# Kernel optimization log

Hardware: AMD Instinct MI355X
Metric: run time of the kernel (lower is better)

Reference implementation:

```python
import jax, jax.numpy as jnp
import numpy as np
import math

B, D, NH, HD, FF, P, IMG = 4, 768, 12, 64, 3072, 16, 256
L = (IMG // P) ** 2      # 256 tokens
PD = P * P * 3           # 768 patch dim
GRID = IMG // P          # 16


def setup_inputs() -> dict:
    key = jax.random.key(0)
    ks = iter(jax.random.split(key, 80))
    def nrm(shape, s=0.02):
        return jax.random.normal(next(ks), shape, jnp.float32) * s
    return {
        "x": jax.random.normal(next(ks), (B, 3, IMG, IMG), jnp.float32),
        "pe_norm_w": jnp.ones((PD,), jnp.float32),
        "pe_proj_w": nrm((PD, D)),
        "pe_proj_b": jnp.zeros((D,), jnp.float32),
        "pe_norm_out_w": jnp.ones((D,), jnp.float32),
        "pos_embed": nrm((1, L, D)),
        "in_attn_norm_w": jnp.ones((6, D), jnp.float32),
        "in_qkv_w": nrm((6, D, 3 * D)),
        "in_out_w": nrm((6, D, D)),
        "in_ff_norm_w": jnp.ones((6, D), jnp.float32),
        "in_w1": nrm((6, D, 2 * FF)),
        "in_w2": nrm((6, FF, D)),
        "mid_attn_norm_w": jnp.ones((3, D), jnp.float32),
        "mid_qkv_w": nrm((3, D, 3 * D)),
        "mid_out_w": nrm((3, D, D)),
        "mid_ff_norm_w": jnp.ones((3, D), jnp.float32),
        "mid_w1": nrm((3, D, 2 * FF)),
        "mid_w2": nrm((3, FF, D)),
        "out_skip_w": nrm((2 * D, D)),
        "out_skip_b": jnp.zeros((D,), jnp.float32),
        "out_attn_norm_w": jnp.ones((D,), jnp.float32),
        "out_qkv_w": nrm((D, 3 * D)),
        "out_out_w": nrm((D, D)),
        "out_ff_norm_w": jnp.ones((D,), jnp.float32),
        "out_w1": nrm((D, 2 * FF)),
        "out_w2": nrm((FF, D)),
        "final_norm_w": jnp.ones((D,), jnp.float32),
        "ol_proj_w": nrm((D, PD)),
        "ol_proj_b": jnp.zeros((PD,), jnp.float32),
        "rb_conv_in_w": nrm((128, 3, 3, 3), 0.1),
        "rb_gn_w": jnp.ones((5, 128), jnp.float32),
        "rb_gn_b": jnp.zeros((5, 128), jnp.float32),
        "rb_conv1_w": nrm((128, 1, 5, 5), 0.1),
        "rb_conv2_w": nrm((128, 1, 5, 5), 0.1),
        "head_conv_w": nrm((1, 128, 3, 3), 0.1),
    }


def _mish(x):
    return x * jnp.tanh(jax.nn.softplus(x))


def _rms(x, w, eps=1e-5):
    return x * jax.lax.rsqrt(jnp.mean(x * x, axis=-1, keepdims=True) + eps) * w


def _attn(x, qkv_w, out_w):
    b, l, _ = x.shape
    q, k, v = jnp.split(x @ qkv_w, 3, axis=-1)
    s = 1.0 / math.sqrt(HD)  # applied to BOTH q and k, as in source
    q = (q * s).reshape(b, l, NH, HD)
    k = (k * s).reshape(b, l, NH, HD)
    v = v.reshape(b, l, NH, HD)
    logits = jnp.einsum('bqhd,bkhd->bhqk', q, k).astype(jnp.float32)
    w = jax.nn.softmax(logits, axis=-1).astype(x.dtype)
    o = jnp.einsum('bhqk,bkhd->bqhd', w, v).reshape(b, l, NH * HD)
    return o @ out_w


def _ff(x, w1, w2):
    a, g = jnp.split(x @ w1, 2, axis=-1)
    return (_mish(a) * g) @ w2


def _block(x, an, qkv, ow, fn, w1, w2):
    x = x + _attn(_rms(x, an), qkv, ow)
    x = x + _ff(_rms(x, fn), w1, w2)
    return x


def _gn(x, w, b, groups=8, eps=1e-5):
    bb, c, h, ww = x.shape
    xg = x.reshape(bb, groups, c // groups, h, ww)
    m = jnp.mean(xg, axis=(2, 3, 4), keepdims=True)
    v = jnp.var(xg, axis=(2, 3, 4), keepdims=True)
    xn = ((xg - m) * jax.lax.rsqrt(v + eps)).reshape(bb, c, h, ww)
    return xn * w[:, None, None] + b[:, None, None]


def _conv(x, w, pad, dil=1, groups=1):
    xp = jnp.pad(x, ((0, 0), (0, 0), (pad, pad), (pad, pad)), mode='reflect')
    return jax.lax.conv_general_dilated(
        xp, w, window_strides=(1, 1), padding='VALID', rhs_dilation=(dil, dil),
        feature_group_count=groups, dimension_numbers=('NCHW', 'OIHW', 'NCHW'))


def _forward(x, pe_norm_w, pe_proj_w, pe_proj_b, pe_norm_out_w, pos_embed,
             in_attn_norm_w, in_qkv_w, in_out_w, in_ff_norm_w, in_w1, in_w2,
             mid_attn_norm_w, mid_qkv_w, mid_out_w, mid_ff_norm_w, mid_w1, mid_w2,
             out_skip_w, out_skip_b, out_attn_norm_w, out_qkv_w, out_out_w,
             out_ff_norm_w, out_w1, out_w2, final_norm_w, ol_proj_w, ol_proj_b,
             rb_conv_in_w, rb_gn_w, rb_gn_b, rb_conv1_w, rb_conv2_w, head_conv_w):
    b = x.shape[0]
    # PatchEmbed: b c (h p1) (w p2) -> b (h w) (p1 p2 c)
    t = x.reshape(b, 3, GRID, P, GRID, P).transpose(0, 2, 4, 3, 5, 1).reshape(b, L, PD)
    t = _rms(t, pe_norm_w)
    t = t @ pe_proj_w + pe_proj_b
    t = _rms(t, pe_norm_out_w)
    t = t + pos_embed
    # U-ViT trunk: 6 in blocks (skips saved), 3 middle, 1 out block (source typo -> single out block)
    skips = []
    for i in range(6):
        t = _block(t, in_attn_norm_w[i], in_qkv_w[i], in_out_w[i],
                   in_ff_norm_w[i], in_w1[i], in_w2[i])
        skips.append(t)
    for i in range(3):
        t = _block(t, mid_attn_norm_w[i], mid_qkv_w[i], mid_out_w[i],
                   mid_ff_norm_w[i], mid_w1[i], mid_w2[i])
    t = jnp.concatenate([t, skips[-1]], axis=-1) @ out_skip_w + out_skip_b
    t = _block(t, out_attn_norm_w, out_qkv_w, out_out_w, out_ff_norm_w, out_w1, out_w2)
    t = _rms(t, final_norm_w)
    # OutBlock: proj, dropout(eval=identity), unpatchify to b 3 256 256
    t = t @ ol_proj_w + ol_proj_b
    img = t.reshape(b, GRID, GRID, P, P, 3).transpose(0, 5, 1, 3, 2, 4).reshape(b, 3, IMG, IMG)
    # ResNetBlock(128)
    h = _conv(img, rb_conv_in_w, 1)
    h = _mish(_gn(h, rb_gn_w[0], rb_gn_b[0]))
    res = h
    h = _mish(_gn(_conv(h, rb_conv1_w, 2, 1, 128), rb_gn_w[1], rb_gn_b[1]))
    h = res + h
    h = _mish(_gn(h, rb_gn_w[2], rb_gn_b[2]))
    res = h
    h = _mish(_gn(_conv(h, rb_conv2_w, 6, 3, 128), rb_gn_w[3], rb_gn_b[3]))
    h = res + h
    h = _mish(_gn(h, rb_gn_w[4], rb_gn_b[4]))
    return _conv(h, head_conv_w, 1)  # [B, 1, 256, 256]


def reference(x, pe_norm_w, pe_proj_w, pe_proj_b, pe_norm_out_w, pos_embed,
              in_attn_norm_w, in_qkv_w, in_out_w, in_ff_norm_w, in_w1, in_w2,
              mid_attn_norm_w, mid_qkv_w, mid_out_w, mid_ff_norm_w, mid_w1, mid_w2,
              out_skip_w, out_skip_b, out_attn_norm_w, out_qkv_w, out_out_w,
              out_ff_norm_w, out_w1, out_w2, final_norm_w, ol_proj_w, ol_proj_b,
              rb_conv_in_w, rb_gn_w, rb_gn_b, rb_conv1_w, rb_conv2_w, head_conv_w):
    return _forward(x, pe_norm_w, pe_proj_w, pe_proj_b, pe_norm_out_w, pos_embed,
                    in_attn_norm_w, in_qkv_w, in_out_w, in_ff_norm_w, in_w1, in_w2,
                    mid_attn_norm_w, mid_qkv_w, mid_out_w, mid_ff_norm_w, mid_w1, mid_w2,
                    out_skip_w, out_skip_b, out_attn_norm_w, out_qkv_w, out_out_w,
                    out_ff_norm_w, out_w1, out_w2, final_norm_w, ol_proj_w, ol_proj_b,
                    rb_conv_in_w, rb_gn_w, rb_gn_b, rb_conv1_w, rb_conv2_w, head_conv_w)
```

## Files before the change

kernel.cpp:

```cpp
#include <hip/hip_runtime.h>
#include <math.h>

#define B_ 4
#define D_ 768
#define NH_ 12
#define HD_ 64
#define FF_ 3072
#define L_ 256
#define PD_ 768
#define GRID_ 16
#define P_ 16
#define IMG_ 256
#define M_ (B_*L_)
#define NCONV_ (B_*128*IMG_*IMG_)

typedef __attribute__((ext_vector_type(8))) short short8;
typedef __attribute__((ext_vector_type(4))) float f32x4;
typedef __attribute__((ext_vector_type(4))) unsigned short us4;
typedef __attribute__((ext_vector_type(8))) unsigned short us8;
typedef unsigned short ushort_t;

__device__ __forceinline__ float mishf(float x){
    float e = __expf(x);
    float u = (1.f + e) * (1.f + e);
    return x * (1.f - 2.f / (u + 1.f));
}

__device__ __forceinline__ int refl(int i, int n){
    if (i < 0) i = -i;
    if (i >= n) i = 2*n - 2 - i;
    return i;
}

__device__ __forceinline__ ushort_t f2bf(float f){
    unsigned int u = __float_as_uint(f);
    unsigned int r = (u + 0x7FFFu + ((u >> 16) & 1u)) >> 16;
    return (ushort_t)r;
}
__device__ __forceinline__ float bf2f(ushort_t u){
    return __uint_as_float(((unsigned int)u) << 16);
}

__device__ __forceinline__ void block_red2(float& s, float& q){
    #pragma unroll
    for (int o = 32; o > 0; o >>= 1){ s += __shfl_down(s, o); q += __shfl_down(q, o); }
    __shared__ float r1[4], r2[4];
    int tid = threadIdx.x;
    if ((tid & 63) == 0){ r1[tid>>6] = s; r2[tid>>6] = q; }
    __syncthreads();
    if (tid == 0){ s = r1[0]+r1[1]+r1[2]+r1[3]; q = r2[0]+r2[1]+r2[2]+r2[3]; }
    __syncthreads();
}

__global__ __launch_bounds__(256) void k_patchify(const float* __restrict__ x, float* __restrict__ t){
    int idx = blockIdx.x*256 + threadIdx.x;
    int d = idx % PD_; int l = (idx/PD_) % L_; int b = idx/(PD_*L_);
    int c = d % 3; int p = d / 3; int p1 = p / P_; int p2 = p % P_;
    int gh = l / GRID_; int gw = l % GRID_;
    int sy = gh*P_ + p1, sx = gw*P_ + p2;
    t[idx] = x[(((size_t)b*3 + c)*IMG_ + sy)*IMG_ + sx];
}

__global__ __launch_bounds__(256) void k_wt(const float* __restrict__ b0, const float* __restrict__ b1,
                                            const float* __restrict__ b2, int n0, int n1,
                                            ushort_t* __restrict__ dst, int K, int N){
    int z = blockIdx.z;
    size_t sz = (size_t)K * N;
    const float* src = (z < n0) ? b0 + (size_t)z*sz
                     : (z < n0+n1) ? b1 + (size_t)(z-n0)*sz
                     : b2 + (size_t)(z-n0-n1)*sz;
    ushort_t* out = dst + (size_t)z*sz;
    __shared__ float ld[32][33];
    int k0 = blockIdx.y*32, nc0 = blockIdx.x*32;
    int tid = threadIdx.x;
    int c = tid & 31, r8 = tid >> 5;
    #pragma unroll
    for (int i = 0; i < 4; ++i){
        int k = r8 + i*8;
        ld[k][c] = src[(size_t)(k0+k)*N + nc0 + c];
    }
    __syncthreads();
    #pragma unroll
    for (int i = 0; i < 4; ++i){
        int n = r8 + i*8;
        out[(size_t)(nc0+n)*K + k0 + c] = f2bf(ld[c][n]);
    }
}

template<bool OUT_BF>
__global__ __launch_bounds__(256) void k_rms(const float* __restrict__ x, const float* __restrict__ w,
                                             const float* __restrict__ addv, void* __restrict__ yv){
    int row = blockIdx.x;
    const float* xr = x + (size_t)row * D_;
    float s = 0.f;
    for (int i = threadIdx.x; i < D_; i += 256){ float v = xr[i]; s += v*v; }
    __shared__ float red[256];
    red[threadIdx.x] = s; __syncthreads();
    for (int o = 128; o > 0; o >>= 1){
        if (threadIdx.x < o) red[threadIdx.x] += red[threadIdx.x+o];
        __syncthreads();
    }
    float rstd = rsqrtf(red[0]/(float)D_ + 1e-5f);
    int l = row % L_;
    for (int i = threadIdx.x; i < D_; i += 256){
        float v = xr[i]*rstd*w[i];
        if (addv) v += addv[(size_t)l*D_ + i];
        if (OUT_BF) ((ushort_t*)yv)[(size_t)row*D_ + i] = f2bf(v);
        else        ((float*)yv)[(size_t)row*D_ + i] = v;
    }
}

__global__ __launch_bounds__(256) void k_skred_rms(const float* __restrict__ Pp, float* __restrict__ t,
                                                   const float* __restrict__ w, ushort_t* __restrict__ nb){
    int row = blockIdx.x;
    int tid = threadIdx.x;
    float v[3];
    float s = 0.f;
    #pragma unroll
    for (int i = 0; i < 3; ++i){
        int c = tid + i*256;
        size_t o = (size_t)row*D_ + c;
        float x = t[o] + Pp[o] + Pp[(size_t)M_*D_ + o];
        v[i] = x; s += x*x;
        t[o] = x;
    }
    #pragma unroll
    for (int o = 32; o > 0; o >>= 1) s += __shfl_down(s, o);
    __shared__ float r1[4];
    if ((tid & 63) == 0) r1[tid>>6] = s;
    __syncthreads();
    float tot = r1[0]+r1[1]+r1[2]+r1[3];
    float rstd = rsqrtf(tot*(1.f/768.f) + 1e-5f);
    if (w){
        #pragma unroll
        for (int i = 0; i < 3; ++i){
            int c = tid + i*256;
            nb[(size_t)row*D_ + c] = f2bf(v[i]*rstd*w[c]);
        }
    }
}

template<bool OBF, int SPLITK>
__global__ __launch_bounds__(256) void k_gemm(const ushort_t* __restrict__ A, const ushort_t* __restrict__ Wt,
                                              void* __restrict__ Cv, const float* __restrict__ bias,
                                              const float* __restrict__ res, int N, int K){
    __shared__ ushort_t As[2][64][40];
    __shared__ ushort_t Ws[2][64][40];
    int tid = threadIdx.x;
    int lane = tid & 63, wid = tid >> 6;
    int wr = wid >> 1, wc = wid & 1;
    int row0 = blockIdx.y * 64, col0 = blockIdx.x * 64;
    f32x4 acc[2][2];
    #pragma unroll
    for (int i = 0; i < 2; ++i)
        #pragma unroll
        for (int j = 0; j < 2; ++j) acc[i][j] = (f32x4){0.f,0.f,0.f,0.f};

    int lg = lane >> 4, lr = lane & 15;
    int sr = tid >> 2, sk = (tid & 3) * 8;
    int kc = K / SPLITK;
    int k0 = (SPLITK > 1) ? blockIdx.z * kc : 0;
    const ushort_t* arow = A  + (size_t)(row0 + sr)*K + k0 + sk;
    const ushort_t* wrow = Wt + (size_t)(col0 + sr)*K + k0 + sk;

    for (int kt = 0; kt < kc; kt += 64){
        __syncthreads();
        *(short8*)&As[0][sr][sk] = *(const short8*)(arow + kt);
        *(short8*)&As[1][sr][sk] = *(const short8*)(arow + kt + 32);
        *(short8*)&Ws[0][sr][sk] = *(const short8*)(wrow + kt);
        *(short8*)&Ws[1][sr][sk] = *(const short8*)(wrow + kt + 32);
        __syncthreads();
        short8 a0[2], a1[2], b0[2], b1[2];
        #pragma unroll
        for (int i = 0; i < 2; ++i){
            a0[i] = *(const short8*)(&As[0][wr*32 + i*16 + lr][lg*8]);
            a1[i] = *(const short8*)(&As[1][wr*32 + i*16 + lr][lg*8]);
        }
        #pragma unroll
        for (int j = 0; j < 2; ++j){
            b0[j] = *(const short8*)(&Ws[0][wc*32 + j*16 + lr][lg*8]);
            b1[j] = *(const short8*)(&Ws[1][wc*32 + j*16 + lr][lg*8]);
        }
        #pragma unroll
        for (int i = 0; i < 2; ++i)
            #pragma unroll
            for (int j = 0; j < 2; ++j){
                acc[i][j] = __builtin_amdgcn_mfma_f32_16x16x32_bf16(a0[i], b0[j], acc[i][j], 0, 0, 0);
                acc[i][j] = __builtin_amdgcn_mfma_f32_16x16x32_bf16(a1[i], b1[j], acc[i][j], 0, 0, 0);
            }
    }
    if (SPLITK > 1){
        float* Pp = (float*)Cv + (size_t)blockIdx.z * M_ * N;
        #pragma unroll
        for (int i = 0; i < 2; ++i)
            #pragma unroll
            for (int j = 0; j < 2; ++j)
                #pragma unroll
                for (int q = 0; q < 4; ++q){
                    int m = row0 + wr*32 + i*16 + lg*4 + q;
                    int n = col0 + wc*32 + j*16 + lr;
                    Pp[(size_t)m*N + n] = acc[i][j][q];
                }
    } else {
        #pragma unroll
        for (int i = 0; i < 2; ++i)
            #pragma unroll
            for (int j = 0; j < 2; ++j)
                #pragma unroll
                for (int q = 0; q < 4; ++q){
                    int m = row0 + wr*32 + i*16 + lg*4 + q;
                    int n = col0 + wc*32 + j*16 + lr;
                    float v = acc[i][j][q];
                    if (bias) v += bias[n];
                    size_t o = (size_t)m*N + n;
                    if (OBF){
                        ((ushort_t*)Cv)[o] = f2bf(v);
                    } else {
                        if (res) v += res[o];
                        ((float*)Cv)[o] = v;
                    }
                }
    }
}

__global__ __launch_bounds__(256) void k_gemm_glu(const ushort_t* __restrict__ A, const ushort_t* __restrict__ Wt,
                                                  ushort_t* __restrict__ Cb, int K){
    __shared__ ushort_t As[2][64][40];
    __shared__ ushort_t Wa[2][64][40];
    __shared__ ushort_t Wg[2][64][40];
    int tid = threadIdx.x;
    int lane = tid & 63, wid = tid >> 6;
    int wr = wid >> 1, wc = wid & 1;
    int row0 = blockIdx.y * 64, col0 = blockIdx.x * 64;
    f32x4 aa[2][2], ag[2][2];
    #pragma unroll
    for (int i = 0; i < 2; ++i)
        #pragma unroll
        for (int j = 0; j < 2; ++j){ aa[i][j] = (f32x4){0.f,0.f,0.f,0.f}; ag[i][j] = (f32x4){0.f,0.f,0.f,0.f}; }

    int lg = lane >> 4, lr = lane & 15;
    int sr = tid >> 2, sk = (tid & 3) * 8;
    const ushort_t* arow = A + (size_t)(row0+sr)*K + sk;
    const ushort_t* war = Wt + (size_t)(col0+sr)*K + sk;
    const ushort_t* wgr = Wt + (size_t)(FF_+col0+sr)*K + sk;

    for (int kt = 0; kt < K; kt += 64){
        __syncthreads();
        *(short8*)&As[0][sr][sk] = *(const short8*)(arow + kt);
        *(short8*)&As[1][sr][sk] = *(const short8*)(arow + kt + 32);
        *(short8*)&Wa[0][sr][sk] = *(const short8*)(war + kt);
        *(short8*)&Wa[1][sr][sk] = *(const short8*)(war + kt + 32);
        *(short8*)&Wg[0][sr][sk] = *(const short8*)(wgr + kt);
        *(short8*)&Wg[1][sr][sk] = *(const short8*)(wgr + kt + 32);
        __syncthreads();
        short8 a0[2], a1[2], ba0[2], ba1[2], bg0[2], bg1[2];
        #pragma unroll
        for (int i = 0; i < 2; ++i){
            a0[i] = *(const short8*)(&As[0][wr*32 + i*16 + lr][lg*8]);
            a1[i] = *(const short8*)(&As[1][wr*32 + i*16 + lr][lg*8]);
        }
        #pragma unroll
        for (int j = 0; j < 2; ++j){
            ba0[j] = *(const short8*)(&Wa[0][wc*32 + j*16 + lr][lg*8]);
            ba1[j] = *(const short8*)(&Wa[1][wc*32 + j*16 + lr][lg*8]);
            bg0[j] = *(const short8*)(&Wg[0][wc*32 + j*16 + lr][lg*8]);
            bg1[j] = *(const short8*)(&Wg[1][wc*32 + j*16 + lr][lg*8]);
        }
        #pragma unroll
        for (int i = 0; i < 2; ++i)
            #pragma unroll
            for (int j = 0; j < 2; ++j){
                aa[i][j] = __builtin_amdgcn_mfma_f32_16x16x32_bf16(a0[i], ba0[j], aa[i][j], 0, 0, 0);
                aa[i][j] = __builtin_amdgcn_mfma_f32_16x16x32_bf16(a1[i], ba1[j], aa[i][j], 0, 0, 0);
                ag[i][j] = __builtin_amdgcn_mfma_f32_16x16x32_bf16(a0[i], bg0[j], ag[i][j], 0, 0, 0);
                ag[i][j] = __builtin_amdgcn_mfma_f32_16x16x32_bf16(a1[i], bg1[j], ag[i][j], 0, 0, 0);
            }
    }
    #pragma unroll
    for (int i = 0; i < 2; ++i)
        #pragma unroll
        for (int j = 0; j < 2; ++j)
            #pragma unroll
            for (int q = 0; q < 4; ++q){
                int m = row0 + wr*32 + i*16 + lg*4 + q;
                int n = col0 + wc*32 + j*16 + lr;
                Cb[(size_t)m*FF_ + n] = f2bf(mishf(aa[i][j][q]) * ag[i][j][q]);
            }
}

__global__ __launch_bounds__(256) void k_attn(const ushort_t* __restrict__ qkv, ushort_t* __restrict__ out){
    int qt = blockIdx.x, h = blockIdx.y, b = blockIdx.z;
    const ushort_t* base = qkv + (size_t)b * L_ * 3 * D_;
    __shared__ ushort_t Qs[64][72];
    __shared__ ushort_t KVs[64][72];
    __shared__ ushort_t Ps[64][268];
    __shared__ float red[8][64];
    int tid = threadIdx.x;
    int lane = tid & 63, w = tid >> 6;
    int lr = lane & 15, lg = lane >> 4;

    {
        int r = tid >> 2, c = (tid & 3) * 16;
        const ushort_t* src = base + (size_t)(qt*64 + r)*3*D_ + h*HD_ + c;
        *(us8*)&Qs[r][c]   = *(const us8*)src;
        *(us8*)&Qs[r][c+8] = *(const us8*)(src + 8);
    }

    f32x4 sacc[4][4];
    #pragma unroll
    for (int kt = 0; kt < 4; ++kt)
        #pragma unroll
        for (int mi = 0; mi < 4; ++mi) sacc[kt][mi] = (f32x4){0.f,0.f,0.f,0.f};

    for (int kt = 0; kt < 4; ++kt){
        __syncthreads();
        {
            int r = tid >> 2, c = (tid & 3) * 16;
            const ushort_t* src = base + (size_t)(kt*64 + r)*3*D_ + D_ + h*HD_ + c;
            *(us8*)&KVs[r][c]   = *(const us8*)src;
            *(us8*)&KVs[r][c+8] = *(const us8*)(src + 8);
        }
        __syncthreads();
        short8 bk0 = *(const short8*)&KVs[w*16 + lr][lg*8];
        short8 bk1 = *(const short8*)&KVs[w*16 + lr][32 + lg*8];
        #pragma unroll
        for (int mi = 0; mi < 4; ++mi){
            short8 a0 = *(const short8*)&Qs[mi*16 + lr][lg*8];
            short8 a1 = *(const short8*)&Qs[mi*16 + lr][32 + lg*8];
            sacc[kt][mi] = __builtin_amdgcn_mfma_f32_16x16x32_bf16(a0, bk0, sacc[kt][mi], 0, 0, 0);
            sacc[kt][mi] = __builtin_amdgcn_mfma_f32_16x16x32_bf16(a1, bk1, sacc[kt][mi], 0, 0, 0);
        }
    }

    const float inv64 = 1.0f/64.0f;
    float gm[4][4], linv[4][4];
    #pragma unroll
    for (int mi = 0; mi < 4; ++mi){
        #pragma unroll
        for (int r = 0; r < 4; ++r){
            float v = fmaxf(fmaxf(sacc[0][mi][r], sacc[1][mi][r]), fmaxf(sacc[2][mi][r], sacc[3][mi][r]));
            v = fmaxf(v, __shfl_xor(v, 1));
            v = fmaxf(v, __shfl_xor(v, 2));
            v = fmaxf(v, __shfl_xor(v, 4));
            v = fmaxf(v, __shfl_xor(v, 8));
            gm[mi][r] = v;
            if (lr == 0) red[w][mi*16 + lg*4 + r] = v;
        }
    }
    __syncthreads();
    #pragma unroll
    for (int mi = 0; mi < 4; ++mi){
        #pragma unroll
        for (int r = 0; r < 4; ++r){
            int row = mi*16 + lg*4 + r;
            float m = fmaxf(fmaxf(red[0][row], red[1][row]), fmaxf(red[2][row], red[3][row]));
            gm[mi][r] = m;
            float sum = 0.f;
            #pragma unroll
            for (int kt = 0; kt < 4; ++kt){
                float p = __expf((sacc[kt][mi][r] - m) * inv64);
                Ps[row][kt*64 + w*16 + lr] = f2bf(p);
                sum += p;
            }
            sum += __shfl_xor(sum, 1);
            sum += __shfl_xor(sum, 2);
            sum += __shfl_xor(sum, 4);
            sum += __shfl_xor(sum, 8);
            linv[mi][r] = sum;
            if (lr == 0) red[4 + w][row] = sum;
        }
    }
    __syncthreads();
    #pragma unroll
    for (int mi = 0; mi < 4; ++mi){
        #pragma unroll
        for (int r = 0; r < 4; ++r){
            int row = mi*16 + lg*4 + r;
            linv[mi][r] = 1.0f / (red[4][row] + red[5][row] + red[6][row] + red[7][row]);
        }
    }

    f32x4 oacc[4];
    #pragma unroll
    for (int mi = 0; mi < 4; ++mi) oacc[mi] = (f32x4){0.f,0.f,0.f,0.f};
    for (int kt = 0; kt < 4; ++kt){
        __syncthreads();
        {
            int k = tid & 63, dg = tid >> 6;
            const ushort_t* src = base + (size_t)(kt*64 + k)*3*D_ + 2*D_ + h*HD_ + dg*16;
            us8 v0 = *(const us8*)src;
            us8 v1 = *(const us8*)(src + 8);
            #pragma unroll
            for (int j = 0; j < 8; ++j) KVs[dg*16 + j][k] = v0[j];
            #pragma unroll
            for (int j = 0; j < 8; ++j) KVs[dg*16 + 8 + j][k] = v1[j];
        }
        __syncthreads();
        short8 bv0 = *(const short8*)&KVs[w*16 + lr][lg*8];
        short8 bv1 = *(const short8*)&KVs[w*16 + lr][32 + lg*8];
        #pragma unroll
        for (int mi = 0; mi < 4; ++mi){
            short8 a0 = *(const short8*)&Ps[mi*16 + lr][kt*64 + lg*8];
            short8 a1 = *(const short8*)&Ps[mi*16 + lr][kt*64 + 32 + lg*8];
            oacc[mi] = __builtin_amdgcn_mfma_f32_16x16x32_bf16(a0, bv0, oacc[mi], 0, 0, 0);
            oacc[mi] = __builtin_amdgcn_mfma_f32_16x16x32_bf16(a1, bv1, oacc[mi], 0, 0, 0);
        }
    }
    #pragma unroll
    for (int mi = 0; mi < 4; ++mi){
        #pragma unroll
        for (int r = 0; r < 4; ++r){
            int row = mi*16 + lg*4 + r;
            out[((size_t)(b*L_ + qt*64 + row))*D_ + h*HD_ + w*16 + lr] = f2bf(oacc[mi][r] * linv[mi][r]);
        }
    }
}

__global__ __launch_bounds__(256) void k_cat(const float* __restrict__ t, const float* __restrict__ skip,
                                             ushort_t* __restrict__ cat){
    int i4 = (blockIdx.x*256 + threadIdx.x) * 4;
    int r = i4 / D_, c = i4 % D_;
    float4 a = *(const float4*)(t + i4);
    float4 b = *(const float4*)(skip + i4);
    us4 ua, ub;
    ua.x=f2bf(a.x); ua.y=f2bf(a.y); ua.z=f2bf(a.z); ua.w=f2bf(a.w);
    ub.x=f2bf(b.x); ub.y=f2bf(b.y); ub.z=f2bf(b.z); ub.w=f2bf(b.w);
    *(us4*)(cat + (size_t)r*1536 + c) = ua;
    *(us4*)(cat + (size_t)r*1536 + 768 + c) = ub;
}

__global__ __launch_bounds__(256) void k_unpatchify(const float* __restrict__ t, float* __restrict__ img){
    int idx = blockIdx.x*256 + threadIdx.x;
    int sx = idx % IMG_; int sy = (idx/IMG_)%IMG_; int c = (idx/(IMG_*IMG_))%3; int b = idx/(3*IMG_*IMG_);
    int gh = sy / P_, p1 = sy % P_, gw = sx / P_, p2 = sx % P_;
    img[idx] = t[(((size_t)b*L_) + gh*GRID_+gw)*PD_ + (p1*P_+p2)*3 + c];
}

__global__ __launch_bounds__(256) void k_conv_in(const float* __restrict__ img, const float* __restrict__ w,
                                                 ushort_t* __restrict__ out, float* __restrict__ partial){
    int y = blockIdx.x, ocg = blockIdx.y, b = blockIdx.z;
    int x = threadIdx.x;
    __shared__ float rows[9][IMG_];
    int yy0 = refl(y-1, IMG_), yy2 = refl(y+1, IMG_);
    #pragma unroll
    for (int ic = 0; ic < 3; ++ic){
        const float* basep = img + ((size_t)(b*3+ic))*IMG_*IMG_;
        rows[ic*3+0][x] = basep[(size_t)yy0*IMG_ + x];
        rows[ic*3+1][x] = basep[(size_t)y  *IMG_ + x];
        rows[ic*3+2][x] = basep[(size_t)yy2*IMG_ + x];
    }
    __syncthreads();
    int xl = (x==0)?1:x-1, xr = (x==255)?254:x+1;
    float sg = 0.f, qg = 0.f;
    for (int oc = ocg*32; oc < ocg*32 + 32; ++oc){
        const float* wv = w + oc*27;
        float acc = 0.f;
        #pragma unroll
        for (int ic = 0; ic < 3; ++ic){
            const float* wk = wv + ic*9;
            acc += rows[ic*3+0][xl]*wk[0] + rows[ic*3+0][x]*wk[1] + rows[ic*3+0][xr]*wk[2]
                 + rows[ic*3+1][xl]*wk[3] + rows[ic*3+1][x]*wk[4] + rows[ic*3+1][xr]*wk[5]
                 + rows[ic*3+2][xl]*wk[6] + rows[ic*3+2][x]*wk[7] + rows[ic*3+2][xr]*wk[8];
        }
        out[(((size_t)(b*128+oc))*IMG_ + y)*IMG_ + x] = f2bf(acc);
        sg += acc; qg += acc*acc;
        if ((oc & 15) == 15){
            block_red2(sg, qg);
            if (threadIdx.x == 0){
                int pidx = ((b*8 + (oc>>4))*256 + y);
                partial[pidx*2] = sg; partial[pidx*2+1] = qg;
            }
            sg = 0.f; qg = 0.f;
        }
    }
}

__global__ __launch_bounds__(256) void k_gn_fin(const float* __restrict__ partial, int nper,
                                                float* __restrict__ stats){
    int bg = blockIdx.x, tid = threadIdx.x;
    float s = 0.f, q = 0.f;
    for (int i = tid; i < nper; i += 256){
        s += partial[((size_t)bg*nper + i)*2];
        q += partial[((size_t)bg*nper + i)*2 + 1];
    }
    block_red2(s, q);
    if (tid == 0){
        const float n = 16.f*IMG_*IMG_;
        float m = s/n;
        float var = q/n - m*m;
        stats[bg*2]   = m;
        stats[bg*2+1] = rsqrtf(var + 1e-5f);
    }
}

__global__ __launch_bounds__(256) void k_act(const ushort_t* __restrict__ x, const float* __restrict__ st,
                                             const float* __restrict__ gw, const float* __restrict__ gb,
                                             ushort_t* __restrict__ y){
    int bid = blockIdx.x;
    int b = bid >> 11, c = (bid >> 4) & 127;
    int bg = b*8 + (c>>4);
    float sc = st[bg*2+1]*gw[c], sb = gb[c] - st[bg*2]*sc;
    size_t e0 = (size_t)bid*4096 + threadIdx.x*16;
    us8 v0 = *(const us8*)(x + e0), v1 = *(const us8*)(x + e0 + 8);
    us8 r0, r1;
    #pragma unroll
    for (int i = 0; i < 8; ++i) r0[i] = f2bf(mishf(bf2f(v0[i])*sc + sb));
    #pragma unroll
    for (int i = 0; i < 8; ++i) r1[i] = f2bf(mishf(bf2f(v1[i])*sc + sb));
    *(us8*)(y + e0) = r0;
    *(us8*)(y + e0 + 8) = r1;
}

template<int PAD, int DIL>
__global__ __launch_bounds__(256) void k_dw(const ushort_t* __restrict__ in,
                                            const float* __restrict__ cw,
                                            ushort_t* __restrict__ out, float* __restrict__ partial){
    constexpr int AP = (DIL==1) ? 4 : 8;
    constexpr int SC = (DIL==1) ? 40 : 48;
    constexpr int SY = 64 + 2*PAD;
    constexpr int CH = SC/4;
    __shared__ float tile[SY*SC];
    int tileid = blockIdx.x, c = blockIdx.y, b = blockIdx.z;
    int x0 = (tileid & 7) * 32, y0 = (tileid >> 3) * 64;
    int tid = threadIdx.x;
    const ushort_t* ip = in + ((size_t)(b*128+c))*IMG_*IMG_;
    int xs = x0 - AP;
    if (xs >= 0 && xs + SC <= IMG_){
        for (int j = tid; j < SY*CH; j += 256){
            int r = j / CH, q = j - r*CH;
            int gy = refl(y0 - PAD + r, IMG_);
            us4 v = *(const us4*)(ip + (size_t)gy*IMG_ + xs + q*4);
            f32x4 fv = { bf2f(v.x), bf2f(v.y), bf2f(v.z), bf2f(v.w) };
            *(f32x4*)&tile[r*SC + q*4] = fv;
        }
    } else {
        for (int j = tid; j < SY*SC; j += 256){
            int r = j / SC, cc = j - r*SC;
            int gy = refl(y0 - PAD + r, IMG_);
            int gx = refl(xs + cc, IMG_);
            tile[r*SC + cc] = bf2f(ip[(size_t)gy*IMG_ + gx]);
        }
    }
    __syncthreads();
    float wreg[25];
    #pragma unroll
    for (int u = 0; u < 25; ++u) wreg[u] = cw[c*25 + u];
    int tx4 = (tid & 7)*4, ty = tid >> 3;
    constexpr int NV = (DIL==1) ? 3 : 5;
    float s = 0.f, q2 = 0.f;
    #pragma unroll
    for (int rr = 0; rr < 2; ++rr){
        int yy = ty + rr*32;
        float acc[4] = {0.f,0.f,0.f,0.f};
        #pragma unroll
        for (int kh = 0; kh < 5; ++kh){
            const float* rowp = &tile[(yy + kh*DIL)*SC + tx4];
            float vv[NV*4];
            #pragma unroll
            for (int u = 0; u < NV; ++u){
                f32x4 v = *(const f32x4*)(rowp + u*4);
                vv[u*4]=v.x; vv[u*4+1]=v.y; vv[u*4+2]=v.z; vv[u*4+3]=v.w;
            }
            #pragma unroll
            for (int kw = 0; kw < 5; ++kw){
                float wk = wreg[kh*5+kw];
                #pragma unroll
                for (int j = 0; j < 4; ++j)
                    acc[j] += vv[kw*DIL + j + (AP - 2*DIL)] * wk;
            }
        }
        us4 o4 = { f2bf(acc[0]), f2bf(acc[1]), f2bf(acc[2]), f2bf(acc[3]) };
        *(us4*)(out + (((size_t)(b*128+c))*IMG_ + y0+yy)*IMG_ + x0+tx4) = o4;
        s  += acc[0]+acc[1]+acc[2]+acc[3];
        q2 += acc[0]*acc[0]+acc[1]*acc[1]+acc[2]*acc[2]+acc[3]*acc[3];
    }
    block_red2(s, q2);
    if (tid == 0){
        int bid = (b*128 + c)*32 + tileid;
        partial[bid*2] = s; partial[bid*2+1] = q2;
    }
}

__global__ __launch_bounds__(256) void k_addmish(const ushort_t* __restrict__ xn, const float* __restrict__ stn,
                                                 const float* __restrict__ wn, const float* __restrict__ bn,
                                                 const ushort_t* __restrict__ resa,
                                                 ushort_t* __restrict__ out, float* __restrict__ partial){
    int bid = blockIdx.x;
    int b = bid >> 11, c = (bid >> 4) & 127;
    int bg = b*8 + (c>>4);
    float scn = stn[bg*2+1]*wn[c], sbn = bn[c] - stn[bg*2]*scn;
    size_t e0 = (size_t)bid*4096 + threadIdx.x*16;
    us8 vn0 = *(const us8*)(xn + e0), vn1 = *(const us8*)(xn + e0 + 8);
    us8 vr0 = *(const us8*)(resa + e0), vr1 = *(const us8*)(resa + e0 + 8);
    us8 r0, r1;
    float s = 0.f, q = 0.f;
    #pragma unroll
    for (int i = 0; i < 8; ++i){
        float v = mishf(bf2f(vn0[i])*scn + sbn) + bf2f(vr0[i]);
        s += v; q += v*v; r0[i] = f2bf(v);
    }
    #pragma unroll
    for (int i = 0; i < 8; ++i){
        float v = mishf(bf2f(vn1[i])*scn + sbn) + bf2f(vr1[i]);
        s += v; q += v*v; r1[i] = f2bf(v);
    }
    *(us8*)(out + e0) = r0;
    *(us8*)(out + e0 + 8) = r1;
    block_red2(s, q);
    if (threadIdx.x == 0){ partial[bid*2] = s; partial[bid*2+1] = q; }
}

__global__ __launch_bounds__(256) void k_head_part(const ushort_t* __restrict__ in, const float* __restrict__ st,
                                                   const float* __restrict__ gw, const float* __restrict__ gb,
                                                   const float* __restrict__ w, float* __restrict__ part){
    __shared__ float tile[34*34];
    int tileid = blockIdx.x, cg = blockIdx.y, b = blockIdx.z;
    int x0 = (tileid & 7)*32, y0 = (tileid >> 3)*32;
    int tid = threadIdx.x;
    int tx4 = (tid & 7)*4, ty = tid >> 3;
    float m  = st[(b*8+cg)*2];
    float rs = st[(b*8+cg)*2 + 1];
    float acc[4] = {0.f,0.f,0.f,0.f};
    for (int ci = 0; ci < 16; ++ci){
        int c = cg*16 + ci;
        float sc = rs*gw[c], sb = gb[c] - m*sc;
        const ushort_t* ip = in + ((size_t)(b*128+c))*IMG_*IMG_;
        if (ci) __syncthreads();
        for (int i = tid; i < 34*34; i += 256){
            int r = i/34, cc = i - r*34;
            int gy = refl(y0-1+r, IMG_);
            int gx = refl(x0-1+cc, IMG_);
            tile[i] = mishf(bf2f(ip[(size_t)gy*IMG_+gx])*sc + sb);
        }
        __syncthreads();
        const float* wc = w + c*9;
        #pragma unroll
        for (int kh = 0; kh < 3; ++kh){
            float vv[6];
            #pragma unroll
            for (int u = 0; u < 6; ++u) vv[u] = tile[(ty+kh)*34 + tx4 + u];
            #pragma unroll
            for (int kw = 0; kw < 3; ++kw){
                float wk = wc[kh*3+kw];
                #pragma unroll
                for (int j = 0; j < 4; ++j) acc[j] += vv[kw+j]*wk;
            }
        }
    }
    f32x4 o = {acc[0], acc[1], acc[2], acc[3]};
    *(f32x4*)(part + (((size_t)(cg*4+b))*IMG_ + y0+ty)*IMG_ + x0+tx4) = o;
}

__global__ __launch_bounds__(256) void k_head_fin(const float* __restrict__ part, float* __restrict__ out){
    int idx4 = blockIdx.x*256 + threadIdx.x;
    size_t e = (size_t)idx4*4;
    int b = (int)(e / (IMG_*IMG_));
    size_t off = e % (IMG_*IMG_);
    f32x4 s = {0.f,0.f,0.f,0.f};
    #pragma unroll
    for (int cg = 0; cg < 8; ++cg){
        f32x4 v = *(const f32x4*)(part + (size_t)(cg*4+b)*IMG_*IMG_ + off);
        s.x += v.x; s.y += v.y; s.z += v.z; s.w += v.w;
    }
    *(f32x4*)(out + e) = s;
}


struct WsMap {
    float *t, *skip, *t2, *ybuf, *img, *partial, *hpart, *stats, *part;
    ushort_t *nb, *qkvb, *ab, *gbuf, *cat, *wb_qkv, *wb_out, *wb_w1, *wb_w2, *wb_pe, *wb_skip, *wb_ol, *cA, *cB;
};

static void run_block(const float* fn, const ushort_t* qw, const ushort_t* ow,
                      const ushort_t* w1, const ushort_t* w2, const float* next_w,
                      float* t, const WsMap& W, hipStream_t stream){
    k_gemm<true,1><<<dim3(3*D_/64, M_/64), 256, 0, stream>>>(W.nb, qw, W.qkvb, nullptr, nullptr, 3*D_, D_);
    k_attn<<<dim3(4, NH_, B_), 256, 0, stream>>>(W.qkvb, W.ab);
    k_gemm<false,1><<<dim3(D_/64, M_/64), 256, 0, stream>>>(W.ab, ow, t, nullptr, t, D_, D_);
    k_rms<true><<<M_, 256, 0, stream>>>(t, fn, nullptr, W.nb);
    k_gemm_glu<<<dim3(FF_/64, M_/64), 256, 0, stream>>>(W.nb, w1, W.gbuf, D_);
    k_gemm<false,2><<<dim3(D_/64, M_/64, 2), 256, 0, stream>>>(W.gbuf, w2, W.part, nullptr, nullptr, D_, FF_);
    k_skred_rms<<<M_, 256, 0, stream>>>(W.part, t, next_w, W.nb);
}

extern "C" void kernel_launch(void* const* d_in, const int* in_sizes, int n_in,
                              void* d_out, int out_size, void* d_ws, size_t ws_size,
                              hipStream_t stream){
    const float* x              = (const float*)d_in[0];
    const float* pe_norm_w      = (const float*)d_in[1];
    const float* pe_proj_w      = (const float*)d_in[2];
    const float* pe_proj_b      = (const float*)d_in[3];
    const float* pe_norm_out_w  = (const float*)d_in[4];
    const float* pos_embed      = (const float*)d_in[5];
    const float* in_attn_norm_w = (const float*)d_in[6];
    const float* in_qkv_w       = (const float*)d_in[7];
    const float* in_out_w       = (const float*)d_in[8];
    const float* in_ff_norm_w   = (const float*)d_in[9];
    const float* in_w1          = (const float*)d_in[10];
    const float* in_w2          = (const float*)d_in[11];
    const float* mid_attn_norm_w= (const float*)d_in[12];
    const float* mid_qkv_w      = (const float*)d_in[13];
    const float* mid_out_w      = (const float*)d_in[14];
    const float* mid_ff_norm_w  = (const float*)d_in[15];
    const float* mid_w1         = (const float*)d_in[16];
    const float* mid_w2         = (const float*)d_in[17];
    const float* out_skip_w     = (const float*)d_in[18];
    const float* out_skip_b     = (const float*)d_in[19];
    const float* out_attn_norm_w= (const float*)d_in[20];
    const float* out_qkv_w      = (const float*)d_in[21];
    const float* out_out_w      = (const float*)d_in[22];
    const float* out_ff_norm_w  = (const float*)d_in[23];
    const float* out_w1         = (const float*)d_in[24];
    const float* out_w2         = (const float*)d_in[25];
    const float* final_norm_w   = (const float*)d_in[26];
    const float* ol_proj_w      = (const float*)d_in[27];
    const float* ol_proj_b      = (const float*)d_in[28];
    const float* rb_conv_in_w   = (const float*)d_in[29];
    const float* rb_gn_w        = (const float*)d_in[30];
    const float* rb_gn_b        = (const float*)d_in[31];
    const float* rb_conv1_w     = (const float*)d_in[32];
    const float* rb_conv2_w     = (const float*)d_in[33];
    const float* head_conv_w    = (const float*)d_in[34];

    WsMap W;
    float* f = (float*)d_ws;
    const size_t TD = (size_t)M_*D_;
    W.t      = f;               f += TD;
    W.skip   = f;               f += TD;
    W.t2     = f;               f += TD;
    W.ybuf   = f;               f += TD;
    W.img    = f;               f += TD;
    W.partial= f;               f += 131072;
    W.hpart  = f;               f += (size_t)8*4*IMG_*IMG_;
    W.stats  = f;               f += 448;
    W.part   = f;               f += (size_t)4*TD;
    ushort_t* u = (ushort_t*)f;
    W.nb     = u;               u += TD;
    W.qkvb   = u;               u += (size_t)M_*3*D_;
    W.ab     = u;               u += TD;
    W.gbuf   = u;               u += (size_t)M_*FF_;
    W.cat    = u;               u += (size_t)M_*2*D_;
    W.wb_qkv = u;               u += (size_t)10*D_*3*D_;
    W.wb_out = u;               u += (size_t)10*D_*D_;
    W.wb_w1  = u;               u += (size_t)10*D_*2*FF_;
    W.wb_w2  = u;               u += (size_t)10*FF_*D_;
    W.wb_pe  = u;               u += (size_t)D_*D_;
    W.wb_skip= u;               u += (size_t)2*D_*D_;
    W.wb_ol  = u;               u += (size_t)D_*D_;
    W.cA     = u;               u += (size_t)NCONV_;
    W.cB     = u;

    float* st0 = W.stats;       float* st1 = W.stats + 64;
    float* st2 = W.stats + 128; float* st3 = W.stats + 192;
    float* st4 = W.stats + 256;

    k_wt<<<dim3(3*D_/32, D_/32, 10), 256, 0, stream>>>(in_qkv_w, mid_qkv_w, out_qkv_w, 6, 3, W.wb_qkv, D_, 3*D_);
    k_wt<<<dim3(D_/32, D_/32, 10), 256, 0, stream>>>(in_out_w, mid_out_w, out_out_w, 6, 3, W.wb_out, D_, D_);
    k_wt<<<dim3(2*FF_/32, D_/32, 10), 256, 0, stream>>>(in_w1, mid_w1, out_w1, 6, 3, W.wb_w1, D_, 2*FF_);
    k_wt<<<dim3(D_/32, FF_/32, 10), 256, 0, stream>>>(in_w2, mid_w2, out_w2, 6, 3, W.wb_w2, FF_, D_);
    k_wt<<<dim3(D_/32, D_/32, 1), 256, 0, stream>>>(pe_proj_w, nullptr, nullptr, 1, 0, W.wb_pe, D_, D_);
    k_wt<<<dim3(D_/32, 2*D_/32, 1), 256, 0, stream>>>(out_skip_w, nullptr, nullptr, 1, 0, W.wb_skip, 2*D_, D_);
    k_wt<<<dim3(D_/32, D_/32, 1), 256, 0, stream>>>(ol_proj_w, nullptr, nullptr, 1, 0, W.wb_ol, D_, D_);

    k_patchify<<<(B_*L_*PD_)/256, 256, 0, stream>>>(x, W.t2);
    k_rms<true><<<M_, 256, 0, stream>>>(W.t2, pe_norm_w, nullptr, W.nb);
    k_gemm<false,1><<<dim3(D_/64, M_/64), 256, 0, stream>>>(W.nb, W.wb_pe, W.t, pe_proj_b, nullptr, D_, D_);
    k_rms<false><<<M_, 256, 0, stream>>>(W.t, pe_norm_out_w, pos_embed, W.t);
    k_rms<true><<<M_, 256, 0, stream>>>(W.t, in_attn_norm_w, nullptr, W.nb);

    for (int i = 0; i < 6; ++i){
        const float* next_w = (i < 5) ? in_attn_norm_w + (size_t)(i+1)*D_ : mid_attn_norm_w;
        run_block(in_ff_norm_w + (size_t)i*D_, W.wb_qkv + (size_t)i*D_*3*D_,
                  W.wb_out + (size_t)i*D_*D_,
                  W.wb_w1 + (size_t)i*D_*2*FF_, W.wb_w2 + (size_t)i*FF_*D_,
                  next_w, W.t, W, stream);
    }
    hipMemcpyAsync(W.skip, W.t, TD*sizeof(float), hipMemcpyDeviceToDevice, stream);

    for (int i = 0; i < 3; ++i){
        int z = 6 + i;
        const float* next_w = (i < 2) ? mid_attn_norm_w + (size_t)(i+1)*D_ : nullptr;
        run_block(mid_ff_norm_w + (size_t)i*D_, W.wb_qkv + (size_t)z*D_*3*D_,
                  W.wb_out + (size_t)z*D_*D_,
                  W.wb_w1 + (size_t)z*D_*2*FF_, W.wb_w2 + (size_t)z*FF_*D_,
                  next_w, W.t, W, stream);
    }

    k_cat<<<(M_*D_)/1024, 256, 0, stream>>>(W.t, W.skip, W.cat);
    k_gemm<false,1><<<dim3(D_/64, M_/64), 256, 0, stream>>>(W.cat, W.wb_skip, W.t2, out_skip_b, nullptr, D_, 2*D_);

    k_rms<true><<<M_, 256, 0, stream>>>(W.t2, out_attn_norm_w, nullptr, W.nb);
    run_block(out_ff_norm_w, W.wb_qkv + (size_t)9*D_*3*D_, W.wb_out + (size_t)9*D_*D_,
              W.wb_w1 + (size_t)9*D_*2*FF_, W.wb_w2 + (size_t)9*FF_*D_,
              final_norm_w, W.t2, W, stream);

    k_gemm<false,1><<<dim3(PD_/64, M_/64), 256, 0, stream>>>(W.nb, W.wb_ol, W.ybuf, ol_proj_b, nullptr, PD_, D_);
    k_unpatchify<<<(B_*3*IMG_*IMG_)/256, 256, 0, stream>>>(W.ybuf, W.img);

    k_conv_in<<<dim3(256, 4, 4), 256, 0, stream>>>(W.img, rb_conv_in_w, W.cA, W.partial);
    k_gn_fin<<<32, 256, 0, stream>>>(W.partial, 256, st0);
    k_act<<<8192, 256, 0, stream>>>(W.cA, st0, rb_gn_w, rb_gn_b, W.cB);
    k_dw<2,1><<<dim3(32, 128, 4), 256, 0, stream>>>(W.cB, rb_conv1_w, W.cA, W.partial);
    k_gn_fin<<<32, 256, 0, stream>>>(W.partial, 512, st1);
    k_addmish<<<8192, 256, 0, stream>>>(W.cA, st1, rb_gn_w+128, rb_gn_b+128, W.cB, W.cA, W.partial);
    k_gn_fin<<<32, 256, 0, stream>>>(W.partial, 256, st2);
    k_act<<<8192, 256, 0, stream>>>(W.cA, st2, rb_gn_w+256, rb_gn_b+256, W.cB);
    k_dw<6,3><<<dim3(32, 128, 4), 256, 0, stream>>>(W.cB, rb_conv2_w, W.cA, W.partial);
    k_gn_fin<<<32, 256, 0, stream>>>(W.partial, 512, st3);
    k_addmish<<<8192, 256, 0, stream>>>(W.cA, st3, rb_gn_w+384, rb_gn_b+384, W.cB, W.cA, W.partial);
    k_gn_fin<<<32, 256, 0, stream>>>(W.partial, 256, st4);
    k_head_part<<<dim3(64, 8, 4), 256, 0, stream>>>(W.cA, st4, rb_gn_w+512, rb_gn_b+512, head_conv_w, W.hpart);
    k_head_fin<<<(B_*IMG_*IMG_)/1024, 256, 0, stream>>>(W.hpart, (float*)d_out);
}
```

Before: 1.522 ms.

## Fuse GroupNorm+Mish activation into depthwise conv load and residual add

Removes the standalone k_act kernels. The GroupNorm affine and Mish are now applied while loading the depthwise-conv tile, and k_addmish recomputes the activated residual from the pre-activation buffer instead of reading a stored activated copy. This drops two full write/read passes over the 4x128x256x256 bf16 tensor. In exchange, Mish is recomputed on halo elements in the conv tiles and a second time in the add kernel, which adds transcendental work.

```diff
diff --git a/kernel.cpp b/kernel.cpp
--- a/kernel.cpp
+++ b/kernel.cpp
@@ -493,26 +493,9 @@
     }
 }
 
-__global__ __launch_bounds__(256) void k_act(const ushort_t* __restrict__ x, const float* __restrict__ st,
-                                             const float* __restrict__ gw, const float* __restrict__ gb,
-                                             ushort_t* __restrict__ y){
-    int bid = blockIdx.x;
-    int b = bid >> 11, c = (bid >> 4) & 127;
-    int bg = b*8 + (c>>4);
-    float sc = st[bg*2+1]*gw[c], sb = gb[c] - st[bg*2]*sc;
-    size_t e0 = (size_t)bid*4096 + threadIdx.x*16;
-    us8 v0 = *(const us8*)(x + e0), v1 = *(const us8*)(x + e0 + 8);
-    us8 r0, r1;
-    #pragma unroll
-    for (int i = 0; i < 8; ++i) r0[i] = f2bf(mishf(bf2f(v0[i])*sc + sb));
-    #pragma unroll
-    for (int i = 0; i < 8; ++i) r1[i] = f2bf(mishf(bf2f(v1[i])*sc + sb));
-    *(us8*)(y + e0) = r0;
-    *(us8*)(y + e0 + 8) = r1;
-}
-
 template<int PAD, int DIL>
-__global__ __launch_bounds__(256) void k_dw(const ushort_t* __restrict__ in,
+__global__ __launch_bounds__(256) void k_dw(const ushort_t* __restrict__ in, const float* __restrict__ st,
+                                            const float* __restrict__ gw, const float* __restrict__ gb,
                                             const float* __restrict__ cw,
                                             ushort_t* __restrict__ out, float* __restrict__ partial){
     constexpr int AP = (DIL==1) ? 4 : 8;
@@ -523,6 +506,9 @@
     int tileid = blockIdx.x, c = blockIdx.y, b = blockIdx.z;
     int x0 = (tileid & 7) * 32, y0 = (tileid >> 3) * 64;
     int tid = threadIdx.x;
+    float m  = st[(b*8 + (c>>4))*2];
+    float rs = st[(b*8 + (c>>4))*2 + 1];
+    float sc = rs*gw[c], sb = gb[c] - m*sc;
     const ushort_t* ip = in + ((size_t)(b*128+c))*IMG_*IMG_;
     int xs = x0 - AP;
     if (xs >= 0 && xs + SC <= IMG_){
@@ -530,7 +516,8 @@
             int r = j / CH, q = j - r*CH;
             int gy = refl(y0 - PAD + r, IMG_);
             us4 v = *(const us4*)(ip + (size_t)gy*IMG_ + xs + q*4);
-            f32x4 fv = { bf2f(v.x), bf2f(v.y), bf2f(v.z), bf2f(v.w) };
+            f32x4 fv = { mishf(bf2f(v.x)*sc + sb), mishf(bf2f(v.y)*sc + sb),
+                         mishf(bf2f(v.z)*sc + sb), mishf(bf2f(v.w)*sc + sb) };
             *(f32x4*)&tile[r*SC + q*4] = fv;
         }
     } else {
@@ -538,7 +525,7 @@
             int r = j / SC, cc = j - r*SC;
             int gy = refl(y0 - PAD + r, IMG_);
             int gx = refl(xs + cc, IMG_);
-            tile[r*SC + cc] = bf2f(ip[(size_t)gy*IMG_ + gx]);
+            tile[r*SC + cc] = mishf(bf2f(ip[(size_t)gy*IMG_ + gx])*sc + sb);
         }
     }
     __syncthreads();
@@ -583,25 +570,27 @@
 
 __global__ __launch_bounds__(256) void k_addmish(const ushort_t* __restrict__ xn, const float* __restrict__ stn,
                                                  const float* __restrict__ wn, const float* __restrict__ bn,
-                                                 const ushort_t* __restrict__ resa,
+                                                 const ushort_t* __restrict__ xo, const float* __restrict__ sto,
+                                                 const float* __restrict__ wo, const float* __restrict__ bo,
                                                  ushort_t* __restrict__ out, float* __restrict__ partial){
     int bid = blockIdx.x;
     int b = bid >> 11, c = (bid >> 4) & 127;
     int bg = b*8 + (c>>4);
     float scn = stn[bg*2+1]*wn[c], sbn = bn[c] - stn[bg*2]*scn;
+    float sco = sto[bg*2+1]*wo[c], sbo = bo[c] - sto[bg*2]*sco;
     size_t e0 = (size_t)bid*4096 + threadIdx.x*16;
     us8 vn0 = *(const us8*)(xn + e0), vn1 = *(const us8*)(xn + e0 + 8);
-    us8 vr0 = *(const us8*)(resa + e0), vr1 = *(const us8*)(resa + e0 + 8);
+    us8 vo0 = *(const us8*)(xo + e0), vo1 = *(const us8*)(xo + e0 + 8);
     us8 r0, r1;
     float s = 0.f, q = 0.f;
     #pragma unroll
     for (int i = 0; i < 8; ++i){
-        float v = mishf(bf2f(vn0[i])*scn + sbn) + bf2f(vr0[i]);
+        float v = mishf(bf2f(vn0[i])*scn + sbn) + mishf(bf2f(vo0[i])*sco + sbo);
         s += v; q += v*v; r0[i] = f2bf(v);
     }
     #pragma unroll
     for (int i = 0; i < 8; ++i){
-        float v = mishf(bf2f(vn1[i])*scn + sbn) + bf2f(vr1[i]);
+        float v = mishf(bf2f(vn1[i])*scn + sbn) + mishf(bf2f(vo1[i])*sco + sbo);
         s += v; q += v*v; r1[i] = f2bf(v);
     }
     *(us8*)(out + e0) = r0;
@@ -799,15 +788,15 @@
 
     k_conv_in<<<dim3(256, 4, 4), 256, 0, stream>>>(W.img, rb_conv_in_w, W.cA, W.partial);
     k_gn_fin<<<32, 256, 0, stream>>>(W.partial, 256, st0);
-    k_act<<<8192, 256, 0, stream>>>(W.cA, st0, rb_gn_w, rb_gn_b, W.cB);
-    k_dw<2,1><<<dim3(32, 128, 4), 256, 0, stream>>>(W.cB, rb_conv1_w, W.cA, W.partial);
+    k_dw<2,1><<<dim3(32, 128, 4), 256, 0, stream>>>(W.cA, st0, rb_gn_w, rb_gn_b, rb_conv1_w, W.cB, W.partial);
     k_gn_fin<<<32, 256, 0, stream>>>(W.partial, 512, st1);
-    k_addmish<<<8192, 256, 0, stream>>>(W.cA, st1, rb_gn_w+128, rb_gn_b+128, W.cB, W.cA, W.partial);
+    k_addmish<<<8192, 256, 0, stream>>>(W.cB, st1, rb_gn_w+128, rb_gn_b+128,
+                                        W.cA, st0, rb_gn_w, rb_gn_b, W.cA, W.partial);
     k_gn_fin<<<32, 256, 0, stream>>>(W.partial, 256, st2);
-    k_act<<<8192, 256, 0, stream>>>(W.cA, st2, rb_gn_w+256, rb_gn_b+256, W.cB);
-    k_dw<6,3><<<dim3(32, 128, 4), 256, 0, stream>>>(W.cB, rb_conv2_w, W.cA, W.partial);
+    k_dw<6,3><<<dim3(32, 128, 4), 256, 0, stream>>>(W.cA, st2, rb_gn_w+256, rb_gn_b+256, rb_conv2_w, W.cB, W.partial);
     k_gn_fin<<<32, 256, 0, stream>>>(W.partial, 512, st3);
-    k_addmish<<<8192, 256, 0, stream>>>(W.cA, st3, rb_gn_w+384, rb_gn_b+384, W.cB, W.cA, W.partial);
+    k_addmish<<<8192, 256, 0, stream>>>(W.cB, st3, rb_gn_w+384, rb_gn_b+384,
+                                        W.cA, st2, rb_gn_w+256, rb_gn_b+256, W.cA, W.partial);
     k_gn_fin<<<32, 256, 0, stream>>>(W.partial, 256, st4);
     k_head_part<<<dim3(64, 8, 4), 256, 0, stream>>>(W.cA, st4, rb_gn_w+512, rb_gn_b+512, head_conv_w, W.hpart);
     k_head_fin<<<(B_*IMG_*IMG_)/1024, 256, 0, stream>>>(W.hpart, (float*)d_out);
```

Result: no change. 1.525 ms (+0.2%).
